# Performance work log

Measured on AMD Instinct MI355X. Metric: run time of the kernel, lower is better.

## Reference

```python
import jax, jax.numpy as jnp
import numpy as np

N = 1024; D = 128; H = 128; FF = 2048; NHEAD = 4; VOCAB = 32000; EPS = 1e-5


def _ln(x, s, b):
    m = x.mean(-1, keepdims=True)
    v = ((x - m) ** 2).mean(-1, keepdims=True)
    return (x - m) / jnp.sqrt(v + EPS) * s + b


def _mha(x, qkv_w, qkv_b, ow, ob):
    n, d = x.shape
    hd = d // NHEAD
    qkv = x @ qkv_w.T + qkv_b  # (n, 3d)
    q, k, v = [t.reshape(n, NHEAD, hd).transpose(1, 0, 2) for t in jnp.split(qkv, 3, axis=-1)]
    scores = jnp.einsum('hqd,hkd->hqk', q, k) / np.float32(np.sqrt(hd))
    attn = jax.nn.softmax(scores, axis=-1)
    o = jnp.einsum('hqk,hkd->hqd', attn, v).transpose(1, 0, 2).reshape(n, d)
    return o @ ow.T + ob


def setup_inputs() -> dict:
    key = jax.random.key(0)
    ks = jax.random.split(key, 10)
    s = 0.02
    p = lambda k, shape: (jax.random.normal(k, shape, jnp.float32) * s)
    return {
        'inputs': jax.random.randint(ks[0], (N,), 0, VOCAB),
        'emb': p(ks[1], (VOCAB, D)),
        'qkv_w': p(ks[2], (2, 3 * D, D)), 'qkv_b': jnp.zeros((2, 3 * D), jnp.float32),
        'attn_out_w': p(ks[3], (2, D, D)), 'attn_out_b': jnp.zeros((2, D), jnp.float32),
        'ln1_s': jnp.ones((2, D), jnp.float32), 'ln1_b': jnp.zeros((2, D), jnp.float32),
        'ln2_s': jnp.ones((2, D), jnp.float32), 'ln2_b': jnp.zeros((2, D), jnp.float32),
        'ff1_w': p(ks[4], (2, FF, D)), 'ff1_b': jnp.zeros((2, FF), jnp.float32),
        'ff2_w': p(ks[5], (2, D, FF)), 'ff2_b': jnp.zeros((2, D), jnp.float32),
        'w1': p(ks[6], (H, 2 * D)), 'b1': jnp.zeros((H,), jnp.float32),
        'w2': p(ks[7], (1, H)), 'b2': jnp.zeros((1,), jnp.float32),
    }


def reference(inputs, emb, qkv_w, qkv_b, attn_out_w, attn_out_b, ln1_s, ln1_b,
              ln2_s, ln2_b, ff1_w, ff1_b, ff2_w, ff2_b, w1, b1, w2, b2):
    x = emb[inputs]  # (n, d)
    for l in range(2):  # post-norm TransformerEncoderLayer (torch default)
        x = _ln(x + _mha(x, qkv_w[l], qkv_b[l], attn_out_w[l], attn_out_b[l]), ln1_s[l], ln1_b[l])
        ff = jax.nn.relu(x @ ff1_w[l].T + ff1_b[l]) @ ff2_w[l].T + ff2_b[l]
        x = _ln(x + ff, ln2_s[l], ln2_b[l])
    # pair MLP: concat(e_i, e_j) @ W1.T == e_i @ W1_left.T + e_j @ W1_right.T
    a = x @ w1[:, :D].T  # (n, H)
    b = x @ w1[:, D:].T  # (n, H)
    h = jax.nn.relu(a[:, None, :] + b[None, :, :] + b1)  # (n, n, H)
    return (h @ w2.T + b2)[..., 0]  # (n, n)
```

## Files before the change

### kernel.cpp

```cpp
#include <hip/hip_runtime.h>
#include <math.h>

#define N_TOK 1024
#define D_MODEL 128
#define NHEAD 4
#define HD 32
#define FF_DIM 2048
#define H_PAIR 128
#define QK_SCALE 0.17677669529663687f

__global__ void embed_kernel(const int* __restrict__ ids, const float* __restrict__ emb,
                             float* __restrict__ x) {
    int u = blockIdx.x * 256 + threadIdx.x;
    int i = u >> 5, d4 = (u & 31) * 4;
    float4 v = *(const float4*)&emb[(size_t)ids[i] * D_MODEL + d4];
    *(float4*)&x[i * D_MODEL + d4] = v;
}

__global__ __launch_bounds__(256) void gemm64(const float* __restrict__ X,
                                              const float* __restrict__ W, int ldw,
                                              const float* __restrict__ bias,
                                              const float* __restrict__ res,
                                              float* __restrict__ C, int M, int Nc, int K,
                                              int act, int kChunk, float* __restrict__ part) {
    __shared__ float Xs[16][68];
    __shared__ float Ws[16][68];
    const int t = threadIdx.x;
    const int tx = t & 15, ty = t >> 4;
    const int m0 = blockIdx.y * 64, n0 = blockIdx.x * 64;
    const int kbase = blockIdx.z * kChunk;

    const int sr = t >> 2;
    const int skq = (t & 3) * 4;
    const float* Xp = X + (size_t)(m0 + sr) * K + kbase + skq;
    const float* Wp = W + (size_t)(n0 + sr) * ldw + kbase + skq;

    float acc[4][4] = {};
    float4 xa = *(const float4*)Xp;
    float4 wa = *(const float4*)Wp;

    for (int k0 = 0; k0 < kChunk; k0 += 16) {
        __syncthreads();
        Xs[skq + 0][sr] = xa.x; Xs[skq + 1][sr] = xa.y;
        Xs[skq + 2][sr] = xa.z; Xs[skq + 3][sr] = xa.w;
        Ws[skq + 0][sr] = wa.x; Ws[skq + 1][sr] = wa.y;
        Ws[skq + 2][sr] = wa.z; Ws[skq + 3][sr] = wa.w;
        __syncthreads();
        if (k0 + 16 < kChunk) {
            xa = *(const float4*)(Xp + k0 + 16);
            wa = *(const float4*)(Wp + k0 + 16);
        }
#pragma unroll
        for (int k = 0; k < 16; ++k) {
            float4 a = *(const float4*)&Xs[k][ty * 4];
            float4 b = *(const float4*)&Ws[k][tx * 4];
            acc[0][0] += a.x * b.x; acc[0][1] += a.x * b.y; acc[0][2] += a.x * b.z; acc[0][3] += a.x * b.w;
            acc[1][0] += a.y * b.x; acc[1][1] += a.y * b.y; acc[1][2] += a.y * b.z; acc[1][3] += a.y * b.w;
            acc[2][0] += a.z * b.x; acc[2][1] += a.z * b.y; acc[2][2] += a.z * b.z; acc[2][3] += a.z * b.w;
            acc[3][0] += a.w * b.x; acc[3][1] += a.w * b.y; acc[3][2] += a.w * b.z; acc[3][3] += a.w * b.w;
        }
    }

    if (part) {
        float* P = part + (size_t)blockIdx.z * M * Nc;
#pragma unroll
        for (int i = 0; i < 4; ++i) {
            int m = m0 + ty * 4 + i;
            *(float4*)&P[(size_t)m * Nc + n0 + tx * 4] =
                make_float4(acc[i][0], acc[i][1], acc[i][2], acc[i][3]);
        }
    } else {
        float4 bv = make_float4(0.f, 0.f, 0.f, 0.f);
        if (bias) bv = *(const float4*)&bias[n0 + tx * 4];
#pragma unroll
        for (int i = 0; i < 4; ++i) {
            int m = m0 + ty * 4 + i;
            float4 v = make_float4(acc[i][0] + bv.x, acc[i][1] + bv.y,
                                   acc[i][2] + bv.z, acc[i][3] + bv.w);
            if (res) {
                float4 rv = *(const float4*)&res[(size_t)m * Nc + n0 + tx * 4];
                v.x += rv.x; v.y += rv.y; v.z += rv.z; v.w += rv.w;
            }
            if (act) {
                v.x = fmaxf(v.x, 0.f); v.y = fmaxf(v.y, 0.f);
                v.z = fmaxf(v.z, 0.f); v.w = fmaxf(v.w, 0.f);
            }
            *(float4*)&C[(size_t)m * Nc + n0 + tx * 4] = v;
        }
    }
}

__global__ __launch_bounds__(256) void attn_flash(const float* __restrict__ qkv,
                                                  float* __restrict__ attn_o) {
    const int h = blockIdx.y;
    const int q0 = blockIdx.x * 16;
    const int t = threadIdx.x;
    const int qi = t & 15;
    const int g = t >> 4;
    __shared__ float Kt[64][36];
    __shared__ float Vt[64][36];
    __shared__ float opart[16][16][36];
    __shared__ float rsum[16][17];

    float qreg[32];
    const float* Qp = qkv + (size_t)(q0 + qi) * 384 + h * HD;
#pragma unroll
    for (int d4 = 0; d4 < 8; ++d4) {
        float4 v = *(const float4*)(Qp + d4 * 4);
        qreg[d4 * 4 + 0] = v.x * QK_SCALE; qreg[d4 * 4 + 1] = v.y * QK_SCALE;
        qreg[d4 * 4 + 2] = v.z * QK_SCALE; qreg[d4 * 4 + 3] = v.w * QK_SCALE;
    }
    float opar[32] = {};
    float psum = 0.f;

    for (int j0 = 0; j0 < N_TOK; j0 += 64) {
        __syncthreads();
#pragma unroll
        for (int u = 0; u < 2; ++u) {
            int uu = t + u * 256;
            int r = uu >> 3, dq = (uu & 7) * 4;
            const float* src = qkv + (size_t)(j0 + r) * 384 + D_MODEL + h * HD + dq;
            float4 kv = *(const float4*)src;
            float4 vv = *(const float4*)(src + D_MODEL);
            *(float4*)&Kt[r][dq] = kv;
            *(float4*)&Vt[r][dq] = vv;
        }
        __syncthreads();
#pragma unroll
        for (int jj = 0; jj < 4; ++jj) {
            const int jl = g * 4 + jj;
            float s = 0.f;
#pragma unroll
            for (int d4 = 0; d4 < 8; ++d4) {
                float4 kv = *(const float4*)&Kt[jl][d4 * 4];
                s += qreg[d4 * 4 + 0] * kv.x + qreg[d4 * 4 + 1] * kv.y
                   + qreg[d4 * 4 + 2] * kv.z + qreg[d4 * 4 + 3] * kv.w;
            }
            float p = __expf(s);
            psum += p;
#pragma unroll
            for (int d4 = 0; d4 < 8; ++d4) {
                float4 vv = *(const float4*)&Vt[jl][d4 * 4];
                opar[d4 * 4 + 0] += p * vv.x; opar[d4 * 4 + 1] += p * vv.y;
                opar[d4 * 4 + 2] += p * vv.z; opar[d4 * 4 + 3] += p * vv.w;
            }
        }
    }

#pragma unroll
    for (int d4 = 0; d4 < 8; ++d4)
        *(float4*)&opart[g][qi][d4 * 4] = make_float4(opar[d4 * 4 + 0], opar[d4 * 4 + 1],
                                                      opar[d4 * 4 + 2], opar[d4 * 4 + 3]);
    rsum[qi][g] = psum;
    __syncthreads();

    {
        const int qi2 = t & 15;
        const int d0 = (t >> 4) * 2;
        float ssum = 0.f;
#pragma unroll
        for (int gg = 0; gg < 16; ++gg) ssum += rsum[qi2][gg];
        float inv = 1.0f / ssum;
        float o0 = 0.f, o1 = 0.f;
#pragma unroll
        for (int gg = 0; gg < 16; ++gg) {
            o0 += opart[gg][qi2][d0];
            o1 += opart[gg][qi2][d0 + 1];
        }
        float* dst = attn_o + (size_t)(q0 + qi2) * D_MODEL + h * HD + d0;
        dst[0] = o0 * inv;
        dst[1] = o1 * inv;
    }
}

__global__ void ln_red(const float* __restrict__ in, int nz, int zstride,
                       const float* __restrict__ bias, const float* __restrict__ res,
                       const float* __restrict__ s, const float* __restrict__ b,
                       float* __restrict__ outp) {
    const int i = blockIdx.x;
    const int t = threadIdx.x;
    float v0 = 0.f, v1 = 0.f;
    for (int z = 0; z < nz; ++z) {
        v0 += in[(size_t)z * zstride + i * 128 + t];
        v1 += in[(size_t)z * zstride + i * 128 + 64 + t];
    }
    if (bias) { v0 += bias[t]; v1 += bias[64 + t]; }
    if (res)  { v0 += res[i * 128 + t]; v1 += res[i * 128 + 64 + t]; }
    float sum = v0 + v1;
    for (int o = 32; o; o >>= 1) sum += __shfl_down(sum, o);
    sum = __shfl(sum, 0);
    float mean = sum * (1.0f / 128.0f);
    float d0 = v0 - mean, d1 = v1 - mean;
    float vs = d0 * d0 + d1 * d1;
    for (int o = 32; o; o >>= 1) vs += __shfl_down(vs, o);
    vs = __shfl(vs, 0);
    float inv = rsqrtf(vs * (1.0f / 128.0f) + 1e-5f);
    outp[i * 128 + t]      = d0 * inv * s[t]      + b[t];
    outp[i * 128 + 64 + t] = d1 * inv * s[64 + t] + b[64 + t];
}

__global__ __launch_bounds__(256) void pair_kernel(const float* __restrict__ A,
                                                   const float* __restrict__ B,
                                                   const float* __restrict__ b1,
                                                   const float* __restrict__ w2,
                                                   const float* __restrict__ b2p,
                                                   float* __restrict__ outp) {
    __shared__ float As[32][132];
    __shared__ float Bs[32][132];
    __shared__ float w2s[128];
    const int t = threadIdx.x;
    const int tx = t & 15, ty = t >> 4;
    const int i0 = blockIdx.y * 32, j0 = blockIdx.x * 32;
    for (int u = t; u < 1024; u += 256) {
        int r = u >> 5, kq = (u & 31) * 4;
        float4 av = *(const float4*)&A[(size_t)(i0 + r) * 128 + kq];
        float4 bb1 = *(const float4*)&b1[kq];
        av.x += bb1.x; av.y += bb1.y; av.z += bb1.z; av.w += bb1.w;
        *(float4*)&As[r][kq] = av;
        *(float4*)&Bs[r][kq] = *(const float4*)&B[(size_t)(j0 + r) * 128 + kq];
    }
    if (t < 32) *(float4*)&w2s[t * 4] = *(const float4*)&w2[t * 4];
    __syncthreads();
    float a00 = 0.f, a01 = 0.f, a10 = 0.f, a11 = 0.f;
#pragma unroll 4
    for (int k4 = 0; k4 < 32; ++k4) {
        float4 x0 = *(const float4*)&As[ty][k4 * 4];
        float4 x1 = *(const float4*)&As[ty + 16][k4 * 4];
        float4 y0 = *(const float4*)&Bs[tx][k4 * 4];
        float4 y1 = *(const float4*)&Bs[tx + 16][k4 * 4];
        float4 w = *(const float4*)&w2s[k4 * 4];
        a00 += fmaxf(x0.x + y0.x, 0.f) * w.x + fmaxf(x0.y + y0.y, 0.f) * w.y
             + fmaxf(x0.z + y0.z, 0.f) * w.z + fmaxf(x0.w + y0.w, 0.f) * w.w;
        a01 += fmaxf(x0.x + y1.x, 0.f) * w.x + fmaxf(x0.y + y1.y, 0.f) * w.y
             + fmaxf(x0.z + y1.z, 0.f) * w.z + fmaxf(x0.w + y1.w, 0.f) * w.w;
        a10 += fmaxf(x1.x + y0.x, 0.f) * w.x + fmaxf(x1.y + y0.y, 0.f) * w.y
             + fmaxf(x1.z + y0.z, 0.f) * w.z + fmaxf(x1.w + y0.w, 0.f) * w.w;
        a11 += fmaxf(x1.x + y1.x, 0.f) * w.x + fmaxf(x1.y + y1.y, 0.f) * w.y
             + fmaxf(x1.z + y1.z, 0.f) * w.z + fmaxf(x1.w + y1.w, 0.f) * w.w;
    }
    float bb = b2p[0];
    outp[(size_t)(i0 + ty) * N_TOK + j0 + tx]            = a00 + bb;
    outp[(size_t)(i0 + ty) * N_TOK + j0 + tx + 16]       = a01 + bb;
    outp[(size_t)(i0 + ty + 16) * N_TOK + j0 + tx]       = a10 + bb;
    outp[(size_t)(i0 + ty + 16) * N_TOK + j0 + tx + 16]  = a11 + bb;
}

extern "C" void kernel_launch(void* const* d_in, const int* in_sizes, int n_in,
                              void* d_out, int out_size, void* d_ws, size_t ws_size,
                              hipStream_t stream) {
    const int*   ids   = (const int*)d_in[0];
    const float* emb   = (const float*)d_in[1];
    const float* qkv_w = (const float*)d_in[2];
    const float* qkv_b = (const float*)d_in[3];
    const float* ow    = (const float*)d_in[4];
    const float* ob    = (const float*)d_in[5];
    const float* ln1_s = (const float*)d_in[6];
    const float* ln1_b = (const float*)d_in[7];
    const float* ln2_s = (const float*)d_in[8];
    const float* ln2_b = (const float*)d_in[9];
    const float* ff1_w = (const float*)d_in[10];
    const float* ff1_b = (const float*)d_in[11];
    const float* ff2_w = (const float*)d_in[12];
    const float* ff2_b = (const float*)d_in[13];
    const float* w1    = (const float*)d_in[14];
    const float* b1    = (const float*)d_in[15];
    const float* w2    = (const float*)d_in[16];
    const float* b2    = (const float*)d_in[17];
    float* out = (float*)d_out;

    float* ws     = (float*)d_ws;
    float* x      = ws;
    float* qkvb   = x + 1024 * 128;
    float* attn_o = qkvb + 1024 * 384;
    float* tmp    = attn_o + 1024 * 128;
    float* ff     = tmp + 1024 * 128;
    float* part   = ff + 1024 * 2048;
    float* pa     = part;
    float* pb     = pa + 1024 * 128;

    embed_kernel<<<128, 256, 0, stream>>>(ids, emb, x);

    for (int l = 0; l < 2; ++l) {
        const float* qw  = qkv_w + l * 384 * 128;
        const float* qb  = qkv_b + l * 384;
        const float* owl = ow + l * 128 * 128;
        const float* obl = ob + l * 128;
        const float* f1w = ff1_w + l * 2048 * 128;
        const float* f1b = ff1_b + l * 2048;
        const float* f2w = ff2_w + l * 128 * 2048;
        const float* f2b = ff2_b + l * 128;

        gemm64<<<dim3(6, 16, 1), 256, 0, stream>>>(x, qw, 128, qb, nullptr, qkvb,
                                                   1024, 384, 128, 0, 128, nullptr);
        attn_flash<<<dim3(64, NHEAD), 256, 0, stream>>>(qkvb, attn_o);
        gemm64<<<dim3(2, 16, 1), 256, 0, stream>>>(attn_o, owl, 128, obl, x, tmp,
                                                   1024, 128, 128, 0, 128, nullptr);
        ln_red<<<1024, 64, 0, stream>>>(tmp, 1, 0, nullptr, nullptr,
                                        ln1_s + l * 128, ln1_b + l * 128, x);
        gemm64<<<dim3(32, 16, 1), 256, 0, stream>>>(x, f1w, 128, f1b, nullptr, ff,
                                                    1024, 2048, 128, 1, 128, nullptr);
        gemm64<<<dim3(2, 16, 8), 256, 0, stream>>>(ff, f2w, 2048, nullptr, nullptr, nullptr,
                                                   1024, 128, 2048, 0, 256, part);
        ln_red<<<1024, 64, 0, stream>>>(part, 8, 1024 * 128, f2b, x,
                                        ln2_s + l * 128, ln2_b + l * 128, x);
    }

    gemm64<<<dim3(2, 16, 1), 256, 0, stream>>>(x, w1, 256, nullptr, nullptr, pa,
                                               1024, 128, 128, 0, 128, nullptr);
    gemm64<<<dim3(2, 16, 1), 256, 0, stream>>>(x, w1 + 128, 256, nullptr, nullptr, pb,
                                               1024, 128, 128, 0, 128, nullptr);
    pair_kernel<<<dim3(32, 32), 256, 0, stream>>>(pa, pb, b1, w2, b2, out);
}
```

Before: 299.7 us.

## Switch encoder GEMMs to bf16 MFMA with bf16 activation copies

```diff
diff --git a/kernel.cpp b/kernel.cpp
--- a/kernel.cpp
+++ b/kernel.cpp
@@ -9,89 +9,108 @@
 #define H_PAIR 128
 #define QK_SCALE 0.17677669529663687f
 
+typedef __attribute__((ext_vector_type(8))) short bf16x8;
+typedef __attribute__((ext_vector_type(4))) float f32x4;
+
+__device__ __forceinline__ unsigned short f2bf(float f) {
+    unsigned u = __float_as_uint(f);
+    u = u + 0x7FFFu + ((u >> 16) & 1u);
+    return (unsigned short)(u >> 16);
+}
+
+__global__ void cvt4_kernel(const float* __restrict__ s0, int n0, const float* __restrict__ s1, int n1,
+                            const float* __restrict__ s2, int n2, const float* __restrict__ s3, int n3,
+                            unsigned short* __restrict__ d0, unsigned short* __restrict__ d1,
+                            unsigned short* __restrict__ d2, unsigned short* __restrict__ d3) {
+    int i = blockIdx.x * 256 + threadIdx.x;
+    if (i < n0) { d0[i] = f2bf(s0[i]); return; } i -= n0;
+    if (i < n1) { d1[i] = f2bf(s1[i]); return; } i -= n1;
+    if (i < n2) { d2[i] = f2bf(s2[i]); return; } i -= n2;
+    if (i < n3) { d3[i] = f2bf(s3[i]); }
+}
+
+__global__ void w1split_kernel(const float* __restrict__ w1, unsigned short* __restrict__ w1L,
+                               unsigned short* __restrict__ w1R) {
+    int h = blockIdx.x, t = threadIdx.x;
+    float v = w1[h * 256 + t];
+    if (t < 128) w1L[h * 128 + t] = f2bf(v);
+    else         w1R[h * 128 + (t - 128)] = f2bf(v);
+}
+
 __global__ void embed_kernel(const int* __restrict__ ids, const float* __restrict__ emb,
-                             float* __restrict__ x) {
+                             float* __restrict__ x, unsigned short* __restrict__ xb) {
     int u = blockIdx.x * 256 + threadIdx.x;
     int i = u >> 5, d4 = (u & 31) * 4;
     float4 v = *(const float4*)&emb[(size_t)ids[i] * D_MODEL + d4];
     *(float4*)&x[i * D_MODEL + d4] = v;
-}
-
-__global__ __launch_bounds__(256) void gemm64(const float* __restrict__ X,
-                                              const float* __restrict__ W, int ldw,
-                                              const float* __restrict__ bias,
-                                              const float* __restrict__ res,
-                                              float* __restrict__ C, int M, int Nc, int K,
-                                              int act, int kChunk, float* __restrict__ part) {
-    __shared__ float Xs[16][68];
-    __shared__ float Ws[16][68];
-    const int t = threadIdx.x;
-    const int tx = t & 15, ty = t >> 4;
-    const int m0 = blockIdx.y * 64, n0 = blockIdx.x * 64;
-    const int kbase = blockIdx.z * kChunk;
-
-    const int sr = t >> 2;
-    const int skq = (t & 3) * 4;
-    const float* Xp = X + (size_t)(m0 + sr) * K + kbase + skq;
-    const float* Wp = W + (size_t)(n0 + sr) * ldw + kbase + skq;
-
-    float acc[4][4] = {};
-    float4 xa = *(const float4*)Xp;
-    float4 wa = *(const float4*)Wp;
-
-    for (int k0 = 0; k0 < kChunk; k0 += 16) {
-        __syncthreads();
-        Xs[skq + 0][sr] = xa.x; Xs[skq + 1][sr] = xa.y;
-        Xs[skq + 2][sr] = xa.z; Xs[skq + 3][sr] = xa.w;
-        Ws[skq + 0][sr] = wa.x; Ws[skq + 1][sr] = wa.y;
-        Ws[skq + 2][sr] = wa.z; Ws[skq + 3][sr] = wa.w;
-        __syncthreads();
-        if (k0 + 16 < kChunk) {
-            xa = *(const float4*)(Xp + k0 + 16);
-            wa = *(const float4*)(Wp + k0 + 16);
-        }
-#pragma unroll
-        for (int k = 0; k < 16; ++k) {
-            float4 a = *(const float4*)&Xs[k][ty * 4];
-            float4 b = *(const float4*)&Ws[k][tx * 4];
-            acc[0][0] += a.x * b.x; acc[0][1] += a.x * b.y; acc[0][2] += a.x * b.z; acc[0][3] += a.x * b.w;
-            acc[1][0] += a.y * b.x; acc[1][1] += a.y * b.y; acc[1][2] += a.y * b.z; acc[1][3] += a.y * b.w;
-            acc[2][0] += a.z * b.x; acc[2][1] += a.z * b.y; acc[2][2] += a.z * b.z; acc[2][3] += a.z * b.w;
-            acc[3][0] += a.w * b.x; acc[3][1] += a.w * b.y; acc[3][2] += a.w * b.z; acc[3][3] += a.w * b.w;
+    ushort4 bv;
+    bv.x = f2bf(v.x); bv.y = f2bf(v.y); bv.z = f2bf(v.z); bv.w = f2bf(v.w);
+    *(ushort4*)&xb[i * D_MODEL + d4] = bv;
+}
+
+__global__ __launch_bounds__(256) void gemm_bf(const unsigned short* __restrict__ Xb,
+                                               const unsigned short* __restrict__ Wb,
+                                               const unsigned short* __restrict__ Wb2,
+                                               const float* __restrict__ bias,
+                                               const float* __restrict__ res,
+                                               float* __restrict__ Cf,
+                                               unsigned short* __restrict__ Cb,
+                                               float* __restrict__ part,
+                                               int M, int Nc, int K, int kChunk, int act) {
+    const int lane = threadIdx.x & 63;
+    const int w = threadIdx.x >> 6;
+    const int m0 = blockIdx.y * 64 + w * 16;
+    const int n0 = blockIdx.x * 64;
+    const int kb = part ? blockIdx.z * kChunk : 0;
+    const int r16 = lane & 15, kh = lane >> 4;
+
+    const unsigned short* Wsel = (Wb2 && blockIdx.z == 1) ? Wb2 : Wb;
+
+    f32x4 acc[4] = {{0.f,0.f,0.f,0.f},{0.f,0.f,0.f,0.f},{0.f,0.f,0.f,0.f},{0.f,0.f,0.f,0.f}};
+    const unsigned short* Ap = Xb + (size_t)(m0 + r16) * K + kb + kh * 8;
+    const unsigned short* Bp = Wsel + (size_t)(n0 + r16) * K + kb + kh * 8;
+
+    for (int k0 = 0; k0 < kChunk; k0 += 32) {
+        bf16x8 a = *(const bf16x8*)(Ap + k0);
+#pragma unroll
+        for (int nt = 0; nt < 4; ++nt) {
+            bf16x8 b = *(const bf16x8*)(Bp + (size_t)nt * 16 * K + k0);
+            acc[nt] = __builtin_amdgcn_mfma_f32_16x16x32_bf16(a, b, acc[nt], 0, 0, 0);
         }
     }
 
     if (part) {
         float* P = part + (size_t)blockIdx.z * M * Nc;
 #pragma unroll
-        for (int i = 0; i < 4; ++i) {
-            int m = m0 + ty * 4 + i;
-            *(float4*)&P[(size_t)m * Nc + n0 + tx * 4] =
-                make_float4(acc[i][0], acc[i][1], acc[i][2], acc[i][3]);
+        for (int nt = 0; nt < 4; ++nt) {
+            int col = n0 + nt * 16 + r16;
+#pragma unroll
+            for (int r = 0; r < 4; ++r) {
+                int row = m0 + kh * 4 + r;
+                P[(size_t)row * Nc + col] = acc[nt][r];
+            }
         }
     } else {
-        float4 bv = make_float4(0.f, 0.f, 0.f, 0.f);
-        if (bias) bv = *(const float4*)&bias[n0 + tx * 4];
-#pragma unroll
-        for (int i = 0; i < 4; ++i) {
-            int m = m0 + ty * 4 + i;
-            float4 v = make_float4(acc[i][0] + bv.x, acc[i][1] + bv.y,
-                                   acc[i][2] + bv.z, acc[i][3] + bv.w);
-            if (res) {
-                float4 rv = *(const float4*)&res[(size_t)m * Nc + n0 + tx * 4];
-                v.x += rv.x; v.y += rv.y; v.z += rv.z; v.w += rv.w;
+        size_t zoff = (size_t)blockIdx.z * M * Nc;
+#pragma unroll
+        for (int nt = 0; nt < 4; ++nt) {
+            int col = n0 + nt * 16 + r16;
+            float bv = bias ? bias[col] : 0.f;
+#pragma unroll
+            for (int r = 0; r < 4; ++r) {
+                int row = m0 + kh * 4 + r;
+                float v = acc[nt][r] + bv;
+                if (res) v += res[(size_t)row * Nc + col];
+                if (act) v = fmaxf(v, 0.f);
+                if (Cf) Cf[zoff + (size_t)row * Nc + col] = v;
+                if (Cb) Cb[zoff + (size_t)row * Nc + col] = f2bf(v);
             }
-            if (act) {
-                v.x = fmaxf(v.x, 0.f); v.y = fmaxf(v.y, 0.f);
-                v.z = fmaxf(v.z, 0.f); v.w = fmaxf(v.w, 0.f);
-            }
-            *(float4*)&C[(size_t)m * Nc + n0 + tx * 4] = v;
         }
     }
 }
 
 __global__ __launch_bounds__(256) void attn_flash(const float* __restrict__ qkv,
-                                                  float* __restrict__ attn_o) {
+                                                  unsigned short* __restrict__ attn_ob) {
     const int h = blockIdx.y;
     const int q0 = blockIdx.x * 16;
     const int t = threadIdx.x;
@@ -167,16 +186,16 @@
             o0 += opart[gg][qi2][d0];
             o1 += opart[gg][qi2][d0 + 1];
         }
-        float* dst = attn_o + (size_t)(q0 + qi2) * D_MODEL + h * HD + d0;
-        dst[0] = o0 * inv;
-        dst[1] = o1 * inv;
+        unsigned short* dst = attn_ob + (size_t)(q0 + qi2) * D_MODEL + h * HD + d0;
+        dst[0] = f2bf(o0 * inv);
+        dst[1] = f2bf(o1 * inv);
     }
 }
 
 __global__ void ln_red(const float* __restrict__ in, int nz, int zstride,
                        const float* __restrict__ bias, const float* __restrict__ res,
                        const float* __restrict__ s, const float* __restrict__ b,
-                       float* __restrict__ outp) {
+                       float* __restrict__ outp, unsigned short* __restrict__ outb) {
     const int i = blockIdx.x;
     const int t = threadIdx.x;
     float v0 = 0.f, v1 = 0.f;
@@ -195,8 +214,12 @@
     for (int o = 32; o; o >>= 1) vs += __shfl_down(vs, o);
     vs = __shfl(vs, 0);
     float inv = rsqrtf(vs * (1.0f / 128.0f) + 1e-5f);
-    outp[i * 128 + t]      = d0 * inv * s[t]      + b[t];
-    outp[i * 128 + 64 + t] = d1 * inv * s[64 + t] + b[64 + t];
+    float r0 = d0 * inv * s[t]      + b[t];
+    float r1 = d1 * inv * s[64 + t] + b[64 + t];
+    outp[i * 128 + t]      = r0;
+    outp[i * 128 + 64 + t] = r1;
+    outb[i * 128 + t]      = f2bf(r0);
+    outb[i * 128 + 64 + t] = f2bf(r1);
 }
 
 __global__ __launch_bounds__(256) void pair_kernel(const float* __restrict__ A,
@@ -268,46 +291,54 @@
     const float* b2    = (const float*)d_in[17];
     float* out = (float*)d_out;
 
-    float* ws     = (float*)d_ws;
-    float* x      = ws;
-    float* qkvb   = x + 1024 * 128;
-    float* attn_o = qkvb + 1024 * 384;
-    float* tmp    = attn_o + 1024 * 128;
-    float* ff     = tmp + 1024 * 128;
-    float* part   = ff + 1024 * 2048;
-    float* pa     = part;
-    float* pb     = pa + 1024 * 128;
-
-    embed_kernel<<<128, 256, 0, stream>>>(ids, emb, x);
+    float* ws = (float*)d_ws;
+    float* x        = ws;
+    unsigned short* xb      = (unsigned short*)(ws + 131072);
+    float* qkvb     = ws + 196608;
+    unsigned short* attn_ob = (unsigned short*)(ws + 589824);
+    float* tmp      = ws + 655360;
+    unsigned short* ffb     = (unsigned short*)(ws + 786432);
+    float* part     = ws + 1835008;
+    float* pab      = ws + 2883584;
+    unsigned short* qkv_wb  = (unsigned short*)(ws + 3145728);
+    unsigned short* owb     = (unsigned short*)(ws + 3194880);
+    unsigned short* ff1b    = (unsigned short*)(ws + 3211264);
+    unsigned short* ff2b    = (unsigned short*)(ws + 3473408);
+    unsigned short* w1L     = (unsigned short*)(ws + 3735552);
+    unsigned short* w1R     = (unsigned short*)(ws + 3743744);
+
+    cvt4_kernel<<<4608, 256, 0, stream>>>(qkv_w, 98304, ow, 32768, ff1_w, 524288,
+                                          ff2_w, 524288, qkv_wb, owb, ff1b, ff2b);
+    w1split_kernel<<<128, 256, 0, stream>>>(w1, w1L, w1R);
+
+    embed_kernel<<<128, 256, 0, stream>>>(ids, emb, x, xb);
 
     for (int l = 0; l < 2; ++l) {
-        const float* qw  = qkv_w + l * 384 * 128;
+        const unsigned short* qwb = qkv_wb + l * 384 * 128;
         const float* qb  = qkv_b + l * 384;
-        const float* owl = ow + l * 128 * 128;
+        const unsigned short* owl = owb + l * 128 * 128;
         const float* obl = ob + l * 128;
-        const float* f1w = ff1_w + l * 2048 * 128;
+        const unsigned short* f1w = ff1b + l * 2048 * 128;
         const float* f1b = ff1_b + l * 2048;
-        const float* f2w = ff2_w + l * 128 * 2048;
+        const unsigned short* f2w = ff2b + l * 128 * 2048;
         const float* f2b = ff2_b + l * 128;
 
-        gemm64<<<dim3(6, 16, 1), 256, 0, stream>>>(x, qw, 128, qb, nullptr, qkvb,
-                                                   1024, 384, 128, 0, 128, nullptr);
-        attn_flash<<<dim3(64, NHEAD), 256, 0, stream>>>(qkvb, attn_o);
-        gemm64<<<dim3(2, 16, 1), 256, 0, stream>>>(attn_o, owl, 128, obl, x, tmp,
-                                                   1024, 128, 128, 0, 128, nullptr);
+        gemm_bf<<<dim3(6, 16, 1), 256, 0, stream>>>(xb, qwb, nullptr, qb, nullptr,
+                                                    qkvb, nullptr, nullptr, 1024, 384, 128, 128, 0);
+        attn_flash<<<dim3(64, NHEAD), 256, 0, stream>>>(qkvb, attn_ob);
+        gemm_bf<<<dim3(2, 16, 1), 256, 0, stream>>>(attn_ob, owl, nullptr, obl, x,
+                                                    tmp, nullptr, nullptr, 1024, 128, 128, 128, 0);
         ln_red<<<1024, 64, 0, stream>>>(tmp, 1, 0, nullptr, nullptr,
-                                        ln1_s + l * 128, ln1_b + l * 128, x);
-        gemm64<<<dim3(32, 16, 1), 256, 0, stream>>>(x, f1w, 128, f1b, nullptr, ff,
-                                                    1024, 2048, 128, 1, 128, nullptr);
-        gemm64<<<dim3(2, 16, 8), 256, 0, stream>>>(ff, f2w, 2048, nullptr, nullptr, nullptr,
-                                                   1024, 128, 2048, 0, 256, part);
+                                        ln1_s + l * 128, ln1_b + l * 128, x, xb);
+        gemm_bf<<<dim3(32, 16, 1), 256, 0, stream>>>(xb, f1w, nullptr, f1b, nullptr,
+                                                     nullptr, ffb, nullptr, 1024, 2048, 128, 128, 1);
+        gemm_bf<<<dim3(2, 16, 8), 256, 0, stream>>>(ffb, f2w, nullptr, nullptr, nullptr,
+                                                    nullptr, nullptr, part, 1024, 128, 2048, 256, 0);
         ln_red<<<1024, 64, 0, stream>>>(part, 8, 1024 * 128, f2b, x,
-                                        ln2_s + l * 128, ln2_b + l * 128, x);
-    }
-
-    gemm64<<<dim3(2, 16, 1), 256, 0, stream>>>(x, w1, 256, nullptr, nullptr, pa,
-                                               1024, 128, 128, 0, 128, nullptr);
-    gemm64<<<dim3(2, 16, 1), 256, 0, stream>>>(x, w1 + 128, 256, nullptr, nullptr, pb,
-                                               1024, 128, 128, 0, 128, nullptr);
-    pair_kernel<<<dim3(32, 32), 256, 0, stream>>>(pa, pb, b1, w2, b2, out);
-}
+                                        ln2_s + l * 128, ln2_b + l * 128, x, xb);
+    }
+
+    gemm_bf<<<dim3(2, 16, 2), 256, 0, stream>>>(xb, w1L, w1R, nullptr, nullptr,
+                                                pab, nullptr, nullptr, 1024, 128, 128, 128, 0);
+    pair_kernel<<<dim3(32, 32), 256, 0, stream>>>(pab, pab + 1024 * 128, b1, w2, b2, out);
+}
```

After: 283.6 us. 1.06x faster.
